# Performance work log

Hardware: AMD Instinct MI355X
Metric: run time of the kernel (lower is better)

## Reference

```python
import jax, jax.numpy as jnp
import numpy as np

N_NODES = 50000
N_EDGES = 800000
D = 64  # in_dim = hidden_dim = out_dim


def gcn_conv(x, edge_index, W, b, num_nodes):
    """PyG GCNConv: x' = D^{-1/2} (A + I) D^{-1/2} (x W) + b."""
    h = x @ W  # [N, out]
    # add self-loops
    loop = jnp.arange(num_nodes, dtype=edge_index.dtype)
    row = jnp.concatenate([edge_index[0], loop])  # sources j
    col = jnp.concatenate([edge_index[1], loop])  # targets i
    # symmetric normalization
    ones = jnp.ones(row.shape[0], dtype=h.dtype)
    deg = jax.ops.segment_sum(ones, col, num_segments=num_nodes)
    dinv = jnp.where(deg > 0, jax.lax.rsqrt(deg), 0.0)
    norm = dinv[row] * dinv[col]  # [E+N]
    # gather -> scale -> scatter-add
    msg = h[row] * norm[:, None]
    out = jax.ops.segment_sum(msg, col, num_segments=num_nodes)
    return out + b


def setup_inputs() -> dict:
    key = jax.random.key(0)
    k = jax.random.split(key, 6)
    x = jax.random.normal(k[0], (N_NODES, D), dtype=jnp.float32)
    edge_index = jax.random.randint(k[1], (2, N_EDGES), 0, N_NODES, dtype=jnp.int64)
    s = 1.0 / np.sqrt(D)
    W1 = jax.random.uniform(k[2], (D, D), jnp.float32, -s, s)
    b1 = jnp.zeros((D,), jnp.float32)
    W2 = jax.random.uniform(k[3], (D, D), jnp.float32, -s, s)
    b2 = jnp.zeros((D,), jnp.float32)
    return {"x": x, "edge_index": edge_index, "W1": W1, "b1": b1, "W2": W2, "b2": b2}


def reference(x, edge_index, W1, b1, W2, b2):
    h = gcn_conv(x, edge_index, W1, b1, N_NODES)
    h = jax.nn.relu(h)
    out = gcn_conv(h, edge_index, W2, b2, N_NODES)
    return out
```

## Files before the change

### kernel.cpp

```cpp
#include <hip/hip_runtime.h>
#include <hip/hip_fp16.h>

#define N_NODES 50000
#define N_EDGES 800000
#define RANGES 8
#define SLICES 16
#define NPB (N_NODES / RANGES)
#define I4S (N_EDGES / SLICES / 4)
#define CAP 48
#define PFX_BLOCKS (N_NODES / 4)
#define GEMM_BLOCKS (N_NODES / 16)

__global__ __launch_bounds__(1024)
void count_kernel(const int* __restrict__ col, unsigned char* __restrict__ cnt8) {
    __shared__ int cur[NPB];
    int tid = threadIdx.x;
    int r = blockIdx.x & (RANGES - 1), s = blockIdx.x >> 3;
    int lo = r * NPB;
    for (int i = tid; i < NPB; i += 1024) cur[i] = 0;
    __syncthreads();
    const int4* c4 = (const int4*)col;
    for (int i = s * I4S + tid; i < (s + 1) * I4S; i += 1024) {
        int4 c = c4[i];
        int dx = c.x - lo, dy = c.y - lo, dz = c.z - lo, dw = c.w - lo;
        if ((unsigned)dx < NPB) atomicAdd(&cur[dx], 1);
        if ((unsigned)dy < NPB) atomicAdd(&cur[dy], 1);
        if ((unsigned)dz < NPB) atomicAdd(&cur[dz], 1);
        if ((unsigned)dw < NPB) atomicAdd(&cur[dw], 1);
    }
    __syncthreads();
    for (int i = tid; i < NPB; i += 1024)
        cnt8[(size_t)s * N_NODES + lo + i] = (unsigned char)min(cur[i], 255);
}

__device__ __forceinline__ float ldf(float v)  { return v; }
__device__ __forceinline__ float ldf(__half v) { return __half2float(v); }

template<typename InT>
__device__ __forceinline__ void gemm_body(int blk, const InT* __restrict__ X,
                                          const float* __restrict__ W,
                                          __half* __restrict__ H) {
    int tid = threadIdx.x, lane = tid & 63, wv = tid >> 6;
    float w[64];
    #pragma unroll
    for (int k = 0; k < 64; ++k) w[k] = W[k * 64 + lane];
    int node0 = blk * 16 + wv * 4;
    #pragma unroll
    for (int r = 0; r < 4; ++r) {
        int node = node0 + r;
        float xv = ldf(X[(size_t)node * 64 + lane]);
        float a0 = 0.f, a1 = 0.f;
        #pragma unroll
        for (int k = 0; k < 64; k += 2) {
            a0 = fmaf(__shfl(xv, k, 64),     w[k],     a0);
            a1 = fmaf(__shfl(xv, k + 1, 64), w[k + 1], a1);
        }
        H[(size_t)node * 64 + lane] = __float2half(a0 + a1);
    }
}

__global__ __launch_bounds__(256)
void prefix_gemm_kernel(const unsigned char* __restrict__ cnt8,
                        unsigned short* __restrict__ base16,
                        int* __restrict__ cntf, float* __restrict__ dinv,
                        unsigned short* __restrict__ dinv16u,
                        const float* __restrict__ X, const float* __restrict__ W,
                        __half* __restrict__ H) {
    if (blockIdx.x < PFX_BLOCKS) {
        int tid = threadIdx.x, lane = tid & 63;
        int node = blockIdx.x * 4 + (tid >> 6);
        int c = 0;
        if (lane < SLICES) c = cnt8[(size_t)lane * N_NODES + node];
        int pin = c;
        #pragma unroll
        for (int off = 1; off < SLICES; off <<= 1) {
            int t = __shfl_up(pin, off, 64);
            if (lane >= off && lane < SLICES) pin += t;
        }
        if (lane < SLICES)
            base16[(size_t)lane * N_NODES + node] = (unsigned short)(pin - c);
        int n = __shfl(pin, SLICES - 1, 64);
        if (lane == 0) {
            float di = rsqrtf((float)(n + 1));
            cntf[node] = min(n, CAP);
            dinv[node] = di;
            dinv16u[node] = __half_as_ushort(__float2half(di));
        }
    } else {
        gemm_body(blockIdx.x - PFX_BLOCKS, X, W, H);
    }
}

__global__ __launch_bounds__(1024)
void place_kernel(const int* __restrict__ row, const int* __restrict__ col,
                  const unsigned short* __restrict__ base16,
                  const unsigned short* __restrict__ dinv16u,
                  unsigned int* __restrict__ epk) {
    __shared__ int cur[NPB];
    int tid = threadIdx.x;
    int r = blockIdx.x & (RANGES - 1), s = blockIdx.x >> 3;
    int lo = r * NPB;
    for (int i = tid; i < NPB; i += 1024)
        cur[i] = base16[(size_t)s * N_NODES + lo + i];
    __syncthreads();
    const int4* c4 = (const int4*)col;
    const int4* r4 = (const int4*)row;
    for (int i = s * I4S + tid; i < (s + 1) * I4S; i += 1024) {
        int4 c  = c4[i];
        int4 rr = r4[i];
        int dx = c.x - lo, dy = c.y - lo, dz = c.z - lo, dw = c.w - lo;
        if ((unsigned)dx < NPB) {
            int p = atomicAdd(&cur[dx], 1);
            if (p < CAP) epk[(size_t)(lo + dx) * CAP + p]
                = (unsigned)rr.x | ((unsigned)dinv16u[rr.x] << 16);
        }
        if ((unsigned)dy < NPB) {
            int p = atomicAdd(&cur[dy], 1);
            if (p < CAP) epk[(size_t)(lo + dy) * CAP + p]
                = (unsigned)rr.y | ((unsigned)dinv16u[rr.y] << 16);
        }
        if ((unsigned)dz < NPB) {
            int p = atomicAdd(&cur[dz], 1);
            if (p < CAP) epk[(size_t)(lo + dz) * CAP + p]
                = (unsigned)rr.z | ((unsigned)dinv16u[rr.z] << 16);
        }
        if ((unsigned)dw < NPB) {
            int p = atomicAdd(&cur[dw], 1);
            if (p < CAP) epk[(size_t)(lo + dw) * CAP + p]
                = (unsigned)rr.w | ((unsigned)dinv16u[rr.w] << 16);
        }
    }
}

template<int MODE>
__global__ __launch_bounds__(256)
void gather_kernel(const __half* __restrict__ H, const int* __restrict__ cntf,
                   const unsigned int* __restrict__ epk,
                   const float* __restrict__ dinv,
                   const float* __restrict__ bias, void* __restrict__ outp) {
    __shared__ float xg[4][64];
    int tid = threadIdx.x, lane = tid & 63, wv = tid >> 6;
    int node = blockIdx.x * 4 + wv;
    int n = cntf[node];
    float di = dinv[node];
    unsigned int e = 0;
    if (lane < n) e = epk[(size_t)node * CAP + lane];
    if (lane == n)
        e = (unsigned)node
          | ((unsigned)__half_as_ushort(__float2half(di)) << 16);
    int m = n + 1;
    int grp = lane >> 3, off = lane & 7;
    const float4* H4 = (const float4*)H;
    float a0=0.f,a1=0.f,a2=0.f,a3=0.f,a4=0.f,a5=0.f,a6=0.f,a7=0.f;
    int nr = (m + 15) & ~15;
    for (int j = 0; j < nr; j += 16) {
        unsigned qa = (unsigned)__shfl((int)e, j + grp, 64);
        unsigned qb = (unsigned)__shfl((int)e, j + 8 + grp, 64);
        float4 va = H4[(size_t)(qa & 0xFFFFu) * 8 + off];
        float4 vb = H4[(size_t)(qb & 0xFFFFu) * 8 + off];
        float wa = __half2float(__ushort_as_half((unsigned short)(qa >> 16)));
        float wb = __half2float(__ushort_as_half((unsigned short)(qb >> 16)));
        const __half2* ha = (const __half2*)&va;
        float2 f0 = __half22float2(ha[0]), f1 = __half22float2(ha[1]);
        float2 f2 = __half22float2(ha[2]), f3 = __half22float2(ha[3]);
        a0 = fmaf(wa, f0.x, a0); a1 = fmaf(wa, f0.y, a1);
        a2 = fmaf(wa, f1.x, a2); a3 = fmaf(wa, f1.y, a3);
        a4 = fmaf(wa, f2.x, a4); a5 = fmaf(wa, f2.y, a5);
        a6 = fmaf(wa, f3.x, a6); a7 = fmaf(wa, f3.y, a7);
        const __half2* hb = (const __half2*)&vb;
        f0 = __half22float2(hb[0]); f1 = __half22float2(hb[1]);
        f2 = __half22float2(hb[2]); f3 = __half22float2(hb[3]);
        a0 = fmaf(wb, f0.x, a0); a1 = fmaf(wb, f0.y, a1);
        a2 = fmaf(wb, f1.x, a2); a3 = fmaf(wb, f1.y, a3);
        a4 = fmaf(wb, f2.x, a4); a5 = fmaf(wb, f2.y, a5);
        a6 = fmaf(wb, f3.x, a6); a7 = fmaf(wb, f3.y, a7);
    }
    a0 += __shfl_xor(a0, 8, 64); a0 += __shfl_xor(a0, 16, 64); a0 += __shfl_xor(a0, 32, 64);
    a1 += __shfl_xor(a1, 8, 64); a1 += __shfl_xor(a1, 16, 64); a1 += __shfl_xor(a1, 32, 64);
    a2 += __shfl_xor(a2, 8, 64); a2 += __shfl_xor(a2, 16, 64); a2 += __shfl_xor(a2, 32, 64);
    a3 += __shfl_xor(a3, 8, 64); a3 += __shfl_xor(a3, 16, 64); a3 += __shfl_xor(a3, 32, 64);
    a4 += __shfl_xor(a4, 8, 64); a4 += __shfl_xor(a4, 16, 64); a4 += __shfl_xor(a4, 32, 64);
    a5 += __shfl_xor(a5, 8, 64); a5 += __shfl_xor(a5, 16, 64); a5 += __shfl_xor(a5, 32, 64);
    a6 += __shfl_xor(a6, 8, 64); a6 += __shfl_xor(a6, 16, 64); a6 += __shfl_xor(a6, 32, 64);
    a7 += __shfl_xor(a7, 8, 64); a7 += __shfl_xor(a7, 16, 64); a7 += __shfl_xor(a7, 32, 64);
    if (lane < 8) {
        xg[wv][lane * 8 + 0] = a0; xg[wv][lane * 8 + 1] = a1;
        xg[wv][lane * 8 + 2] = a2; xg[wv][lane * 8 + 3] = a3;
        xg[wv][lane * 8 + 4] = a4; xg[wv][lane * 8 + 5] = a5;
        xg[wv][lane * 8 + 6] = a6; xg[wv][lane * 8 + 7] = a7;
    }
    float sum = xg[wv][lane];
    float res = di * sum + bias[lane];
    if constexpr (MODE == 0) {
        ((__half*)outp)[(size_t)node * 64 + lane] = __float2half(fmaxf(res, 0.f));
    } else {
        ((float*)outp)[(size_t)node * 64 + lane] = res;
    }
}

__global__ __launch_bounds__(256)
void gemm2_kernel(const __half* __restrict__ G, const float* __restrict__ W,
                  __half* __restrict__ H) {
    gemm_body(blockIdx.x, G, W, H);
}

extern "C" void kernel_launch(void* const* d_in, const int* in_sizes, int n_in,
                              void* d_out, int out_size, void* d_ws, size_t ws_size,
                              hipStream_t stream) {
    const float* x   = (const float*)d_in[0];
    const int*   ei  = (const int*)d_in[1];
    const int*   row = ei;
    const int*   col = ei + N_EDGES;
    const float* W1  = (const float*)d_in[2];
    const float* b1  = (const float*)d_in[3];
    const float* W2  = (const float*)d_in[4];
    const float* b2  = (const float*)d_in[5];
    float* out = (float*)d_out;

    char* p = (char*)d_ws;
    __half* h  = (__half*)p;            p += (size_t)N_NODES * 64 * 2;
    __half* g  = (__half*)p;            p += (size_t)N_NODES * 64 * 2;
    unsigned char*  cnt8    = (unsigned char*)p;  p += (size_t)SLICES * N_NODES;
    unsigned short* base16  = (unsigned short*)p; p += (size_t)SLICES * N_NODES * 2;
    unsigned int*   epk     = (unsigned int*)p;   p += (size_t)N_NODES * CAP * 4;
    float*          dinv    = (float*)p;          p += (size_t)N_NODES * 4;
    unsigned short* dinv16u = (unsigned short*)p; p += (size_t)N_NODES * 2;
    int*            cntf    = (int*)p;            p += (size_t)N_NODES * 4;

    count_kernel<<<RANGES * SLICES, 1024, 0, stream>>>(col, cnt8);
    prefix_gemm_kernel<<<PFX_BLOCKS + GEMM_BLOCKS, 256, 0, stream>>>(
        cnt8, base16, cntf, dinv, dinv16u, x, W1, h);
    place_kernel<<<RANGES * SLICES, 1024, 0, stream>>>(row, col, base16, dinv16u, epk);
    gather_kernel<0><<<N_NODES / 4, 256, 0, stream>>>(h, cntf, epk, dinv, b1, g);
    gemm2_kernel<<<GEMM_BLOCKS, 256, 0, stream>>>(g, W2, h);
    gather_kernel<1><<<N_NODES / 4, 256, 0, stream>>>(h, cntf, epk, dinv, b2, out);
}
```

Measured before the change: 241.9 us.

## Fuse second GEMM into first gather and compute slice prefixes on the fly

Transposes the per-slice count table to node-major so each node's sixteen counts are one 16-byte load. The separate prefix pass and base16 buffer are removed: degree sums are computed in a small dinv pass and each place block derives its slice offset from the byte counts. The layer-2 GEMM is fused into the epilogue of the first gather, which drops one kernel launch and one round trip of the intermediate activations through memory. In exchange, each gather wave now loads 64 W2 values into registers, which may lower occupancy.

```diff
diff --git a/kernel.cpp b/kernel.cpp
--- a/kernel.cpp
+++ b/kernel.cpp
@@ -8,8 +8,8 @@
 #define NPB (N_NODES / RANGES)
 #define I4S (N_EDGES / SLICES / 4)
 #define CAP 48
-#define PFX_BLOCKS (N_NODES / 4)
 #define GEMM_BLOCKS (N_NODES / 16)
+#define DINV_BLOCKS ((N_NODES + 255) / 256)
 
 __global__ __launch_bounds__(1024)
 void count_kernel(const int* __restrict__ col, unsigned char* __restrict__ cnt8) {
@@ -30,14 +30,10 @@
     }
     __syncthreads();
     for (int i = tid; i < NPB; i += 1024)
-        cnt8[(size_t)s * N_NODES + lo + i] = (unsigned char)min(cur[i], 255);
-}
-
-__device__ __forceinline__ float ldf(float v)  { return v; }
-__device__ __forceinline__ float ldf(__half v) { return __half2float(v); }
-
-template<typename InT>
-__device__ __forceinline__ void gemm_body(int blk, const InT* __restrict__ X,
+        cnt8[(size_t)(lo + i) * SLICES + s] = (unsigned char)min(cur[i], 255);
+}
+
+__device__ __forceinline__ void gemm_body(int blk, const float* __restrict__ X,
                                           const float* __restrict__ W,
                                           __half* __restrict__ H) {
     int tid = threadIdx.x, lane = tid & 63, wv = tid >> 6;
@@ -48,7 +44,7 @@
     #pragma unroll
     for (int r = 0; r < 4; ++r) {
         int node = node0 + r;
-        float xv = ldf(X[(size_t)node * 64 + lane]);
+        float xv = X[(size_t)node * 64 + lane];
         float a0 = 0.f, a1 = 0.f;
         #pragma unroll
         for (int k = 0; k < 64; k += 2) {
@@ -59,49 +55,53 @@
     }
 }
 
+__device__ __forceinline__ int bytesum4(unsigned v) {
+    return (v & 0xFF) + ((v >> 8) & 0xFF) + ((v >> 16) & 0xFF) + (v >> 24);
+}
+
 __global__ __launch_bounds__(256)
-void prefix_gemm_kernel(const unsigned char* __restrict__ cnt8,
-                        unsigned short* __restrict__ base16,
-                        int* __restrict__ cntf, float* __restrict__ dinv,
-                        unsigned short* __restrict__ dinv16u,
-                        const float* __restrict__ X, const float* __restrict__ W,
-                        __half* __restrict__ H) {
-    if (blockIdx.x < PFX_BLOCKS) {
-        int tid = threadIdx.x, lane = tid & 63;
-        int node = blockIdx.x * 4 + (tid >> 6);
-        int c = 0;
-        if (lane < SLICES) c = cnt8[(size_t)lane * N_NODES + node];
-        int pin = c;
-        #pragma unroll
-        for (int off = 1; off < SLICES; off <<= 1) {
-            int t = __shfl_up(pin, off, 64);
-            if (lane >= off && lane < SLICES) pin += t;
-        }
-        if (lane < SLICES)
-            base16[(size_t)lane * N_NODES + node] = (unsigned short)(pin - c);
-        int n = __shfl(pin, SLICES - 1, 64);
-        if (lane == 0) {
+void gemm_dinv_kernel(const unsigned char* __restrict__ cnt8,
+                      int* __restrict__ cntf, float* __restrict__ dinv,
+                      unsigned short* __restrict__ dinv16u,
+                      const float* __restrict__ X, const float* __restrict__ W,
+                      __half* __restrict__ H) {
+    if (blockIdx.x < GEMM_BLOCKS) {
+        gemm_body(blockIdx.x, X, W, H);
+    } else {
+        int node = (blockIdx.x - GEMM_BLOCKS) * 256 + threadIdx.x;
+        if (node < N_NODES) {
+            uint4 c = ((const uint4*)cnt8)[node];
+            int n = bytesum4(c.x) + bytesum4(c.y) + bytesum4(c.z) + bytesum4(c.w);
             float di = rsqrtf((float)(n + 1));
             cntf[node] = min(n, CAP);
             dinv[node] = di;
             dinv16u[node] = __half_as_ushort(__float2half(di));
         }
-    } else {
-        gemm_body(blockIdx.x - PFX_BLOCKS, X, W, H);
     }
 }
 
 __global__ __launch_bounds__(1024)
 void place_kernel(const int* __restrict__ row, const int* __restrict__ col,
-                  const unsigned short* __restrict__ base16,
+                  const unsigned char* __restrict__ cnt8,
                   const unsigned short* __restrict__ dinv16u,
                   unsigned int* __restrict__ epk) {
     __shared__ int cur[NPB];
     int tid = threadIdx.x;
     int r = blockIdx.x & (RANGES - 1), s = blockIdx.x >> 3;
     int lo = r * NPB;
-    for (int i = tid; i < NPB; i += 1024)
-        cur[i] = base16[(size_t)s * N_NODES + lo + i];
+    for (int i = tid; i < NPB; i += 1024) {
+        uint4 c = ((const uint4*)cnt8)[lo + i];
+        unsigned w0 = c.x, w1 = c.y, w2 = c.z, w3 = c.w;
+        int base = 0;
+        if (s >= 4)  { base += bytesum4(w0); }
+        else         { for (int k = 0; k < s; ++k)      base += (w0 >> (8*k)) & 0xFF; }
+        if (s >= 8)  { base += bytesum4(w1); }
+        else if (s > 4)  { for (int k = 0; k < s-4; ++k)  base += (w1 >> (8*k)) & 0xFF; }
+        if (s >= 12) { base += bytesum4(w2); }
+        else if (s > 8)  { for (int k = 0; k < s-8; ++k)  base += (w2 >> (8*k)) & 0xFF; }
+        if (s > 12)  { for (int k = 0; k < s-12; ++k) base += (w3 >> (8*k)) & 0xFF; }
+        cur[i] = base;
+    }
     __syncthreads();
     const int4* c4 = (const int4*)col;
     const int4* r4 = (const int4*)row;
@@ -132,12 +132,13 @@
     }
 }
 
-template<int MODE>
+template<int FUSE>
 __global__ __launch_bounds__(256)
 void gather_kernel(const __half* __restrict__ H, const int* __restrict__ cntf,
                    const unsigned int* __restrict__ epk,
                    const float* __restrict__ dinv,
-                   const float* __restrict__ bias, void* __restrict__ outp) {
+                   const float* __restrict__ bias, const float* __restrict__ W2,
+                   void* __restrict__ outp) {
     __shared__ float xg[4][64];
     int tid = threadIdx.x, lane = tid & 63, wv = tid >> 6;
     int node = blockIdx.x * 4 + wv;
@@ -190,18 +191,22 @@
         xg[wv][lane * 8 + 6] = a6; xg[wv][lane * 8 + 7] = a7;
     }
     float sum = xg[wv][lane];
-    float res = di * sum + bias[lane];
-    if constexpr (MODE == 0) {
-        ((__half*)outp)[(size_t)node * 64 + lane] = __float2half(fmaxf(res, 0.f));
+    float gval = di * sum + bias[lane];
+    if constexpr (FUSE) {
+        gval = fmaxf(gval, 0.f);
+        float wc[64];
+        #pragma unroll
+        for (int k = 0; k < 64; ++k) wc[k] = W2[k * 64 + lane];
+        float o0 = 0.f, o1 = 0.f;
+        #pragma unroll
+        for (int k = 0; k < 64; k += 2) {
+            o0 = fmaf(__shfl(gval, k, 64),     wc[k],     o0);
+            o1 = fmaf(__shfl(gval, k + 1, 64), wc[k + 1], o1);
+        }
+        ((__half*)outp)[(size_t)node * 64 + lane] = __float2half(o0 + o1);
     } else {
-        ((float*)outp)[(size_t)node * 64 + lane] = res;
-    }
-}
-
-__global__ __launch_bounds__(256)
-void gemm2_kernel(const __half* __restrict__ G, const float* __restrict__ W,
-                  __half* __restrict__ H) {
-    gemm_body(blockIdx.x, G, W, H);
+        ((float*)outp)[(size_t)node * 64 + lane] = gval;
+    }
 }
 
 extern "C" void kernel_launch(void* const* d_in, const int* in_sizes, int n_in,
@@ -219,19 +224,17 @@
 
     char* p = (char*)d_ws;
     __half* h  = (__half*)p;            p += (size_t)N_NODES * 64 * 2;
-    __half* g  = (__half*)p;            p += (size_t)N_NODES * 64 * 2;
-    unsigned char*  cnt8    = (unsigned char*)p;  p += (size_t)SLICES * N_NODES;
-    unsigned short* base16  = (unsigned short*)p; p += (size_t)SLICES * N_NODES * 2;
+    __half* h2 = (__half*)p;            p += (size_t)N_NODES * 64 * 2;
+    unsigned char*  cnt8    = (unsigned char*)p;  p += (size_t)N_NODES * SLICES;
     unsigned int*   epk     = (unsigned int*)p;   p += (size_t)N_NODES * CAP * 4;
     float*          dinv    = (float*)p;          p += (size_t)N_NODES * 4;
     unsigned short* dinv16u = (unsigned short*)p; p += (size_t)N_NODES * 2;
     int*            cntf    = (int*)p;            p += (size_t)N_NODES * 4;
 
     count_kernel<<<RANGES * SLICES, 1024, 0, stream>>>(col, cnt8);
-    prefix_gemm_kernel<<<PFX_BLOCKS + GEMM_BLOCKS, 256, 0, stream>>>(
-        cnt8, base16, cntf, dinv, dinv16u, x, W1, h);
-    place_kernel<<<RANGES * SLICES, 1024, 0, stream>>>(row, col, base16, dinv16u, epk);
-    gather_kernel<0><<<N_NODES / 4, 256, 0, stream>>>(h, cntf, epk, dinv, b1, g);
-    gemm2_kernel<<<GEMM_BLOCKS, 256, 0, stream>>>(g, W2, h);
-    gather_kernel<1><<<N_NODES / 4, 256, 0, stream>>>(h, cntf, epk, dinv, b2, out);
-}
+    gemm_dinv_kernel<<<GEMM_BLOCKS + DINV_BLOCKS, 256, 0, stream>>>(
+        cnt8, cntf, dinv, dinv16u, x, W1, h);
+    place_kernel<<<RANGES * SLICES, 1024, 0, stream>>>(row, col, cnt8, dinv16u, epk);
+    gather_kernel<1><<<N_NODES / 4, 256, 0, stream>>>(h, cntf, epk, dinv, b1, W2, h2);
+    gather_kernel<0><<<N_NODES / 4, 256, 0, stream>>>(h2, cntf, epk, dinv, b2, nullptr, out);
+}
```

Result: faster. 219.7 us (-9.2%).
